# Kernel tuning notes

Hardware: AMD Instinct MI355X
Metric: run time of the kernel (lower is better)

Reference implementation:

```python
import jax, jax.numpy as jnp
from jax import lax
import numpy as np

T = 3          # num_frame
DIV = 2        # channel_shift div
PAD = 1        # kernel_size//2 (same padding for k=3)


def setup_inputs() -> dict:
    key = jax.random.key(0)
    k1, k2 = jax.random.split(key)
    x = jax.random.normal(k1, (12, 64, 256, 256), dtype=jnp.float32)      # (B*T, C, H, W)
    weight = jax.random.normal(k2, (64, 64, 3, 3), dtype=jnp.float32)     # (O, I, kh, kw)
    return {"x": x, "weight": weight}


def reference(x, weight):
    BT, C, H, W = x.shape
    B = BT // T
    # channel_shift: view (B, T*C, H, W), roll by C//div along channel axis
    shift = C // DIV
    y = x.reshape(B, T * C, H, W)
    y = jnp.roll(y, shift, axis=1).reshape(BT, C, H, W)
    # BinaryConv2d: sign(activations), sign(weights) * per-out-channel mean|W|
    scale = jnp.mean(jnp.abs(weight), axis=(1, 2, 3), keepdims=True)      # (O,1,1,1)
    bw = jnp.sign(weight) * scale
    bx = jnp.sign(y)
    out = lax.conv_general_dilated(
        bx, bw,
        window_strides=(1, 1),
        padding=[(PAD, PAD), (PAD, PAD)],
        dimension_numbers=("NCHW", "OIHW", "NCHW"),
    )
    return out
```

## Files before the change

kernel.cpp:

```cpp
#include <hip/hip_runtime.h>
#include <stdint.h>

typedef unsigned long long u64;
typedef unsigned int u32;

#define HW 65536
#define WD 256

__global__ __launch_bounds__(64) void pack_w_kernel(const float* __restrict__ wt,
                                                    u64* __restrict__ pw,
                                                    float* __restrict__ scale) {
    const int o = blockIdx.x;
    const int i = threadIdx.x;
    const float* p = wt + o * 576 + i * 9;
    float v[9];
    float s = 0.f;
#pragma unroll
    for (int k = 0; k < 9; k++) { v[k] = p[k]; s += fabsf(v[k]); }
#pragma unroll
    for (int k = 0; k < 9; k++) {
        u64 m = __ballot((__float_as_uint(v[k]) >> 31) != 0u);
        if (i == 0) pw[o * 9 + k] = m;
    }
#pragma unroll
    for (int off = 32; off > 0; off >>= 1) s += __shfl_down(s, off);
    if (i == 0) scale[o] = s * (1.0f / 576.0f);
}

__global__ __launch_bounds__(256) void pack_x_kernel(const float* __restrict__ x,
                                                     u64* __restrict__ px) {
    const int n = blockIdx.x >> 6;
    const int s = ((blockIdx.x & 63) << 10) + (threadIdx.x << 2);
    const int b = n / 3;
    const int t = n - b * 3;
    const int fp = b * 3 + (t + 2) % 3;

    const float* xa = x + ((size_t)fp * 64 + 32) * HW + s;
    const float* xb = x + (size_t)n * 64 * HW + s;

    u32 lo0 = 0, lo1 = 0, lo2 = 0, lo3 = 0;
    u32 hi0 = 0, hi1 = 0, hi2 = 0, hi3 = 0;
#pragma unroll
    for (int c = 0; c < 32; c++) {
        float4 va = *(const float4*)(xa + (size_t)c * HW);
        lo0 |= (__float_as_uint(va.x) >> 31) << c;
        lo1 |= (__float_as_uint(va.y) >> 31) << c;
        lo2 |= (__float_as_uint(va.z) >> 31) << c;
        lo3 |= (__float_as_uint(va.w) >> 31) << c;
        float4 vb = *(const float4*)(xb + (size_t)c * HW);
        hi0 |= (__float_as_uint(vb.x) >> 31) << c;
        hi1 |= (__float_as_uint(vb.y) >> 31) << c;
        hi2 |= (__float_as_uint(vb.z) >> 31) << c;
        hi3 |= (__float_as_uint(vb.w) >> 31) << c;
    }
    u64* dst = px + (size_t)n * HW + s;
    dst[0] = ((u64)hi0 << 32) | lo0;
    dst[1] = ((u64)hi1 << 32) | lo1;
    dst[2] = ((u64)hi2 << 32) | lo2;
    dst[3] = ((u64)hi3 << 32) | lo3;
}

__global__ __launch_bounds__(256) void bconv_kernel(const u64* __restrict__ px,
                                                    const u64* __restrict__ pw,
                                                    const float* __restrict__ scale,
                                                    float* __restrict__ out) {
    const int w = (blockIdx.x << 6) + (threadIdx.x & 63);
    const int h = (blockIdx.y << 2) + (threadIdx.x >> 6);
    const int n = blockIdx.z;
    const u64* base = px + (size_t)n * HW;

    const bool edge_block = (blockIdx.x == 0) | (blockIdx.x == 3) |
                            (blockIdx.y == 0) | (blockIdx.y == 63);

    u64 xv[9];
    float* op = out + (size_t)n * 64 * HW + h * WD + w;

    if (!edge_block) {
#pragma unroll
        for (int dh = -1; dh <= 1; dh++)
#pragma unroll
            for (int dw = -1; dw <= 1; dw++)
                xv[(dh + 1) * 3 + (dw + 1)] = base[(h + dh) * WD + (w + dw)];

#pragma unroll 4
        for (int o = 0; o < 64; o++) {
            const u64* wp = pw + o * 9;
            int cnt = 0;
#pragma unroll
            for (int k = 0; k < 9; k++) cnt += __popcll(xv[k] ^ wp[k]);
            const float sc = scale[o];
            __builtin_nontemporal_store(fmaf(-2.f * sc, (float)cnt, 576.f * sc),
                                        op + (size_t)o * HW);
        }
    } else {
        u64 mk[9];
        int ninv = 0;
#pragma unroll
        for (int dh = -1; dh <= 1; dh++) {
#pragma unroll
            for (int dw = -1; dw <= 1; dw++) {
                const int k = (dh + 1) * 3 + (dw + 1);
                const int hh = h + dh, ww = w + dw;
                const bool valid = (hh >= 0) && (hh < 256) && (ww >= 0) && (ww < 256);
                const int hc = min(max(hh, 0), 255);
                const int wc = min(max(ww, 0), 255);
                xv[k] = base[hc * WD + wc];
                mk[k] = valid ? ~0ull : 0ull;
                ninv += valid ? 0 : 1;
            }
        }
        const int basecnt = 32 * ninv;

#pragma unroll 4
        for (int o = 0; o < 64; o++) {
            const u64* wp = pw + o * 9;
            int cnt = basecnt;
#pragma unroll
            for (int k = 0; k < 9; k++) cnt += __popcll((xv[k] ^ wp[k]) & mk[k]);
            const float sc = scale[o];
            __builtin_nontemporal_store(fmaf(-2.f * sc, (float)cnt, 576.f * sc),
                                        op + (size_t)o * HW);
        }
    }
}

extern "C" void kernel_launch(void* const* d_in, const int* in_sizes, int n_in,
                              void* d_out, int out_size, void* d_ws, size_t ws_size,
                              hipStream_t stream) {
    (void)in_sizes; (void)n_in; (void)out_size; (void)ws_size;
    const float* x  = (const float*)d_in[0];
    const float* wt = (const float*)d_in[1];
    float* out = (float*)d_out;

    u64* px = (u64*)d_ws;
    u64* pw = px + (size_t)12 * HW;
    float* scale = (float*)(pw + 576);

    pack_w_kernel<<<64, 64, 0, stream>>>(wt, pw, scale);
    pack_x_kernel<<<768, 256, 0, stream>>>(x, px);
    bconv_kernel<<<dim3(4, 64, 12), 256, 0, stream>>>(px, pw, scale, out);
}
```

Before: 384.7 us.

## Compute four pixels per thread in bconv and split border handling into separate kernel

The main binary conv kernel now has each thread compute four adjacent output columns from a 3x6 register window of packed words. This reuses input loads and weight words across pixels and issues 16-byte nontemporal stores. Border pixels are handled by a new dedicated edge kernel that overwrites them with masked results, which removes the edge branch from the main kernel. The pack kernel also switches to nontemporal vector loads and 16-byte stores. Both conv kernels write the border pixels, so correctness depends on the edge kernel running after the main one in stream order.

```diff
diff --git a/kernel.cpp b/kernel.cpp
--- a/kernel.cpp
+++ b/kernel.cpp
@@ -3,6 +3,8 @@
 
 typedef unsigned long long u64;
 typedef unsigned int u32;
+typedef float f32x4 __attribute__((ext_vector_type(4)));
+typedef u64 u64x2 __attribute__((ext_vector_type(2)));
 
 #define HW 65536
 #define WD 256
@@ -35,92 +37,121 @@
     const int t = n - b * 3;
     const int fp = b * 3 + (t + 2) % 3;
 
-    const float* xa = x + ((size_t)fp * 64 + 32) * HW + s;
-    const float* xb = x + (size_t)n * 64 * HW + s;
+    const f32x4* xa = (const f32x4*)(x + ((size_t)fp * 64 + 32) * HW + s);
+    const f32x4* xb = (const f32x4*)(x + (size_t)n * 64 * HW + s);
 
     u32 lo0 = 0, lo1 = 0, lo2 = 0, lo3 = 0;
     u32 hi0 = 0, hi1 = 0, hi2 = 0, hi3 = 0;
 #pragma unroll
     for (int c = 0; c < 32; c++) {
-        float4 va = *(const float4*)(xa + (size_t)c * HW);
+        f32x4 va = __builtin_nontemporal_load(xa + c * (HW / 4));
         lo0 |= (__float_as_uint(va.x) >> 31) << c;
         lo1 |= (__float_as_uint(va.y) >> 31) << c;
         lo2 |= (__float_as_uint(va.z) >> 31) << c;
         lo3 |= (__float_as_uint(va.w) >> 31) << c;
-        float4 vb = *(const float4*)(xb + (size_t)c * HW);
+        f32x4 vb = __builtin_nontemporal_load(xb + c * (HW / 4));
         hi0 |= (__float_as_uint(vb.x) >> 31) << c;
         hi1 |= (__float_as_uint(vb.y) >> 31) << c;
         hi2 |= (__float_as_uint(vb.z) >> 31) << c;
         hi3 |= (__float_as_uint(vb.w) >> 31) << c;
     }
     u64* dst = px + (size_t)n * HW + s;
-    dst[0] = ((u64)hi0 << 32) | lo0;
-    dst[1] = ((u64)hi1 << 32) | lo1;
-    dst[2] = ((u64)hi2 << 32) | lo2;
-    dst[3] = ((u64)hi3 << 32) | lo3;
+    u64x2 d01 = { ((u64)hi0 << 32) | lo0, ((u64)hi1 << 32) | lo1 };
+    u64x2 d23 = { ((u64)hi2 << 32) | lo2, ((u64)hi3 << 32) | lo3 };
+    *(u64x2*)(dst)     = d01;
+    *(u64x2*)(dst + 2) = d23;
 }
 
 __global__ __launch_bounds__(256) void bconv_kernel(const u64* __restrict__ px,
                                                     const u64* __restrict__ pw,
                                                     const float* __restrict__ scale,
                                                     float* __restrict__ out) {
-    const int w = (blockIdx.x << 6) + (threadIdx.x & 63);
-    const int h = (blockIdx.y << 2) + (threadIdx.x >> 6);
-    const int n = blockIdx.z;
+    const int g  = threadIdx.x & 63;
+    const int w4 = g << 2;
+    const int h  = (blockIdx.x << 2) + (threadIdx.x >> 6);
+    const int n  = blockIdx.y;
     const u64* base = px + (size_t)n * HW;
 
-    const bool edge_block = (blockIdx.x == 0) | (blockIdx.x == 3) |
-                            (blockIdx.y == 0) | (blockIdx.y == 63);
+    u64 W[3][6];
+#pragma unroll
+    for (int r = 0; r < 3; r++) {
+        const int hh = min(max(h - 1 + r, 0), 255);
+        const u64* row = base + hh * WD;
+        W[r][0] = row[max(w4 - 1, 0)];
+#pragma unroll
+        for (int k = 1; k < 5; k++) W[r][k] = row[w4 - 1 + k];
+        W[r][5] = row[min(w4 + 4, 255)];
+    }
 
-    u64 xv[9];
-    float* op = out + (size_t)n * 64 * HW + h * WD + w;
-
-    if (!edge_block) {
-#pragma unroll
-        for (int dh = -1; dh <= 1; dh++)
-#pragma unroll
-            for (int dw = -1; dw <= 1; dw++)
-                xv[(dh + 1) * 3 + (dw + 1)] = base[(h + dh) * WD + (w + dw)];
+    float* op = out + (size_t)n * 64 * HW + h * WD + w4;
 
 #pragma unroll 4
-        for (int o = 0; o < 64; o++) {
-            const u64* wp = pw + o * 9;
-            int cnt = 0;
+    for (int o = 0; o < 64; o++) {
+        const u64* wp = pw + o * 9;
+        int c0 = 0, c1 = 0, c2 = 0, c3 = 0;
 #pragma unroll
-            for (int k = 0; k < 9; k++) cnt += __popcll(xv[k] ^ wp[k]);
-            const float sc = scale[o];
-            __builtin_nontemporal_store(fmaf(-2.f * sc, (float)cnt, 576.f * sc),
-                                        op + (size_t)o * HW);
-        }
-    } else {
-        u64 mk[9];
-        int ninv = 0;
+        for (int r = 0; r < 3; r++) {
 #pragma unroll
-        for (int dh = -1; dh <= 1; dh++) {
-#pragma unroll
-            for (int dw = -1; dw <= 1; dw++) {
-                const int k = (dh + 1) * 3 + (dw + 1);
-                const int hh = h + dh, ww = w + dw;
-                const bool valid = (hh >= 0) && (hh < 256) && (ww >= 0) && (ww < 256);
-                const int hc = min(max(hh, 0), 255);
-                const int wc = min(max(ww, 0), 255);
-                xv[k] = base[hc * WD + wc];
-                mk[k] = valid ? ~0ull : 0ull;
-                ninv += valid ? 0 : 1;
+            for (int dw = 0; dw < 3; dw++) {
+                const u64 t = wp[r * 3 + dw];
+                c0 += __popcll(W[r][0 + dw] ^ t);
+                c1 += __popcll(W[r][1 + dw] ^ t);
+                c2 += __popcll(W[r][2 + dw] ^ t);
+                c3 += __popcll(W[r][3 + dw] ^ t);
             }
         }
-        const int basecnt = 32 * ninv;
+        const float sc = scale[o];
+        const float b  = 576.f * sc, m = -2.f * sc;
+        f32x4 v = { fmaf(m, (float)c0, b), fmaf(m, (float)c1, b),
+                    fmaf(m, (float)c2, b), fmaf(m, (float)c3, b) };
+        __builtin_nontemporal_store(v, (f32x4*)(op + (size_t)o * HW));
+    }
+}
 
-#pragma unroll 4
-        for (int o = 0; o < 64; o++) {
-            const u64* wp = pw + o * 9;
-            int cnt = basecnt;
+__global__ __launch_bounds__(256) void bconv_edge_kernel(const u64* __restrict__ px,
+                                                         const u64* __restrict__ pw,
+                                                         const float* __restrict__ scale,
+                                                         float* __restrict__ out) {
+    const int idx = (blockIdx.x << 8) + threadIdx.x;
+    const int p   = idx >> 3;
+    const int og  = (idx & 7) << 3;
+    const int n   = blockIdx.y;
+    if (p >= 1020) return;
+
+    int h, w;
+    if (p < 256)      { h = 0;       w = p;       }
+    else if (p < 512) { h = 255;     w = p - 256; }
+    else if (p < 766) { w = 0;       h = p - 511; }
+    else              { w = 255;     h = p - 765; }
+
+    const u64* base = px + (size_t)n * HW;
+    u64 xv[9];
+    u64 mk[9];
+    int ninv = 0;
 #pragma unroll
-            for (int k = 0; k < 9; k++) cnt += __popcll((xv[k] ^ wp[k]) & mk[k]);
-            const float sc = scale[o];
-            __builtin_nontemporal_store(fmaf(-2.f * sc, (float)cnt, 576.f * sc),
-                                        op + (size_t)o * HW);
+    for (int dh = -1; dh <= 1; dh++) {
+#pragma unroll
+        for (int dw = -1; dw <= 1; dw++) {
+            const int k = (dh + 1) * 3 + (dw + 1);
+            const int hh = h + dh, ww = w + dw;
+            const bool valid = (hh >= 0) && (hh < 256) && (ww >= 0) && (ww < 256);
+            xv[k] = base[min(max(hh, 0), 255) * WD + min(max(ww, 0), 255)];
+            mk[k] = valid ? ~0ull : 0ull;
+            ninv += valid ? 0 : 1;
         }
+    }
+    const int basecnt = 32 * ninv;
+
+    float* op = out + (size_t)n * 64 * HW + h * WD + w;
+#pragma unroll
+    for (int j = 0; j < 8; j++) {
+        const int o = og + j;
+        const u64* wp = pw + o * 9;
+        int cnt = basecnt;
+#pragma unroll
+        for (int k = 0; k < 9; k++) cnt += __popcll((xv[k] ^ wp[k]) & mk[k]);
+        const float sc = scale[o];
+        op[(size_t)o * HW] = fmaf(-2.f * sc, (float)cnt, 576.f * sc);
     }
 }
 
@@ -138,5 +169,6 @@
 
     pack_w_kernel<<<64, 64, 0, stream>>>(wt, pw, scale);
     pack_x_kernel<<<768, 256, 0, stream>>>(x, px);
-    bconv_kernel<<<dim3(4, 64, 12), 256, 0, stream>>>(px, pw, scale, out);
+    bconv_kernel<<<dim3(64, 12), 256, 0, stream>>>(px, pw, scale, out);
+    bconv_edge_kernel<<<dim3(32, 12), 256, 0, stream>>>(px, pw, scale, out);
 }
```

After: 388.8 us. No clear change (+1.1%).
